# Optimization experiments

Measured on AMD Instinct MI355X. Metric: run time of the kernel, lower is better.

The kernel has to match this reference:

```python
import jax, jax.numpy as jnp
import numpy as np

N_NODES = 50000
N_EDGES = 625000
IN_CH = 128
OUT_CH = 128


def setup_inputs() -> dict:
    key = jax.random.key(0)
    k1, k2, k3, k4 = jax.random.split(key, 4)
    x = jax.random.normal(k1, (N_NODES, IN_CH), dtype=jnp.float32)
    edge_index = jax.random.randint(k2, (2, N_EDGES), 0, N_NODES, dtype=jnp.int64)
    # nn.Linear(in, out): weight [out, in], bias [out]
    bound = 1.0 / np.sqrt(IN_CH)
    W = jax.random.uniform(k3, (OUT_CH, IN_CH), minval=-bound, maxval=bound, dtype=jnp.float32)
    b = jax.random.uniform(k4, (OUT_CH,), minval=-bound, maxval=bound, dtype=jnp.float32)
    return {"x": x, "edge_index": edge_index, "W": W, "b": b}


def reference(x, edge_index, W, b):
    row, col = edge_index[0], edge_index[1]
    num_nodes = x.shape[0]
    # degree of destination nodes (scatter_add of ones over row)
    deg = jax.ops.segment_sum(jnp.ones(row.shape[0], dtype=x.dtype), row,
                              num_segments=num_nodes)
    deg_inv_sqrt = jnp.where(deg > 0, jax.lax.rsqrt(jnp.maximum(deg, 1.0)) * jnp.where(deg > 0, 1.0, 0.0), 0.0)
    deg_inv_sqrt = jnp.where(deg > 0, deg ** -0.5, 0.0)
    norm = deg_inv_sqrt[row] * deg_inv_sqrt[col]  # [E]
    src = x[col] * norm[:, None]                  # gather + scale, [E, C]
    out = jax.ops.segment_sum(src, row, num_segments=num_nodes)  # scatter-add
    return out @ W.T + b
```

## Files before the change

kernel.cpp:

```cpp
#include <hip/hip_runtime.h>
#include <hip/hip_bf16.h>

#define NN 50000
#define NE 625000
#define CH 128
#define RSTR 32
#define NG 196
#define NBIN 512
#define EPB 1221

typedef __attribute__((ext_vector_type(8))) short short8;
typedef __attribute__((ext_vector_type(4))) float floatx4;

__device__ __forceinline__ ushort f2bf(float v) {
    __hip_bfloat16 h = __float2bfloat16(v);
    return *(ushort*)&h;
}
__device__ __forceinline__ float bf2f(uint u) {
    return __uint_as_float(u << 16);
}

__global__ __launch_bounds__(256) void k_prep(const float* __restrict__ x,
                                              ushort* __restrict__ xb,
                                              const float* __restrict__ W,
                                              ushort* __restrict__ whi,
                                              ushort* __restrict__ wlo,
                                              const int* __restrict__ row,
                                              const int* __restrict__ col,
                                              uint* __restrict__ runtbl,
                                              uint* __restrict__ gseg) {
    __shared__ uint cnt[NG];
    __shared__ uint sc[NG];
    __shared__ uint ss[256];
    __shared__ uint pk[EPB];

    int b = blockIdx.x;
    int t = threadIdx.x;
    if (b < NBIN) {
        int e0 = b * EPB;
        int n = NE - e0; if (n > EPB) n = EPB;

        for (int i = t; i < NG; i += 256) cnt[i] = 0;
        __syncthreads();

        int r[5], c[5], g[5];
        uint rk[5];
#pragma unroll
        for (int j = 0; j < 5; ++j) {
            int i = t + j * 256;
            int idx = (i < n) ? (e0 + i) : e0;
            r[j] = row[idx];
            c[j] = col[idx];
        }
#pragma unroll
        for (int j = 0; j < 5; ++j) {
            g[j] = r[j] >> 8;
            if (t + j * 256 < n) rk[j] = atomicAdd(&cnt[g[j]], 1u);
        }
        __syncthreads();

        ss[t] = (t < NG) ? cnt[t] : 0u;
        __syncthreads();
        for (int off = 1; off < 256; off <<= 1) {
            uint add = (t >= off) ? ss[t - off] : 0u;
            __syncthreads();
            ss[t] += add;
            __syncthreads();
        }
        if (t < NG) {
            sc[t] = ss[t] - cnt[t];
            runtbl[(size_t)t * NBIN + b] = (sc[t] << 12) | cnt[t];
        }
        __syncthreads();

#pragma unroll
        for (int j = 0; j < 5; ++j) {
            if (t + j * 256 < n) {
                uint pos = sc[g[j]] + rk[j];
                pk[pos] = ((uint)(r[j] & 255) << 16) | (uint)(c[j] & 0xffff);
            }
        }
        __syncthreads();

        for (int i = t; i < n; i += 256)
            gseg[e0 + i] = pk[i];
    } else if (b < 6762) {
        int i = ((b - 512) * 256 + t) * 4;
        float4 v = *(const float4*)(x + i);
        ushort4 o;
        o.x = f2bf(v.x); o.y = f2bf(v.y); o.z = f2bf(v.z); o.w = f2bf(v.w);
        *(ushort4*)(xb + i) = o;
    } else {
        int i = (b - 6762) * 256 + t;
        float v = W[i];
        ushort hh = f2bf(v);
        whi[i] = hh;
        wlo[i] = f2bf(v - bf2f((uint)hh));
    }
}

__global__ __launch_bounds__(256) void k_csr(const uint* __restrict__ gseg,
                                             const uint* __restrict__ runtbl,
                                             uint* __restrict__ csr,
                                             int* __restrict__ deg_c,
                                             float* __restrict__ nrm) {
    __shared__ ushort slots[64][62];
    __shared__ uint dcnt[64];
    __shared__ uint rt[NBIN];
    int g = blockIdx.x >> 2;
    int q = blockIdx.x & 3;
    int t = threadIdx.x;

    if (t < 64) dcnt[t] = 0;
    for (int i = t; i < NBIN; i += 256)
        rt[i] = runtbl[(size_t)g * NBIN + i];
    __syncthreads();

#pragma unroll
    for (int rep = 0; rep < NBIN / 256; ++rep) {
        int bb = t + rep * 256;
        uint d = rt[bb];
        uint s = d >> 12, len = d & 0xFFFu;
        const uint* p = gseg + (size_t)bb * EPB + s;
        for (uint k = 0; k < len; ++k) {
            uint e = p[k];
            int rl = (int)(e >> 16);
            if ((rl >> 6) == q) {
                int r6 = rl & 63;
                uint kk = atomicAdd(&dcnt[r6], 1u);
                if (kk < 62) slots[r6][kk] = (ushort)(e & 0xffff);
            }
        }
    }
    __syncthreads();

    int row0 = g * 256 + q * 64;
    for (int i = t; i < 2048; i += 256) {
        int rl = i >> 5, w = i & 31;
        int rr = row0 + rl;
        if (rr < NN) {
            uint val;
            if (w == 0) val = dcnt[rl];
            else val = (uint)slots[rl][2 * w - 2] | ((uint)slots[rl][2 * w - 1] << 16);
            csr[(size_t)rr * RSTR + w] = val;
        }
    }
    if (t < 64) {
        int rr = row0 + t;
        if (rr < NN) {
            int d = (int)dcnt[t];
            deg_c[rr] = d;
            nrm[rr] = (d > 0) ? rsqrtf((float)d) : 0.0f;
        }
    }
}

__global__ __launch_bounds__(256) void k_aggm(const ushort* __restrict__ xb,
                                              const int* __restrict__ deg_c,
                                              const float* __restrict__ nrm,
                                              const uint* __restrict__ csr,
                                              const ushort* __restrict__ whi,
                                              const ushort* __restrict__ wlo,
                                              const float* __restrict__ bias,
                                              float* __restrict__ out) {
    __shared__ ushort at[32 * 128];
    const int wave = threadIdx.x >> 6;
    const int lane = threadIdx.x & 63;
    const int half = lane >> 5;
    const int lq = lane & 31;
    const int m0 = blockIdx.x * 32;
    const int li = (lane < 62) ? lane : 0;

    int node0 = m0 + wave * 8;
    int deg_n = 0; ushort craw_n = 0; float dr_n = 0.0f;
    if (node0 < NN) {
        deg_n  = deg_c[node0];
        craw_n = ((const ushort*)(csr + (size_t)node0 * RSTR))[2 + li];
        dr_n   = nrm[node0];
    }
    for (int s = 0; s < 8; ++s) {
        int node = node0 + s;
        int r = wave * 8 + s;
        if (node >= NN) {
            if (half == 0) {
                int byte = (r * 256 + lq * 8) ^ ((r & 7) << 4);
                *(uint2*)((char*)at + byte) = make_uint2(0u, 0u);
            }
            continue;
        }
        int deg = deg_n; ushort craw = craw_n; float dr = dr_n;
        int cli = (lane < deg) ? (int)craw : 0;
        float nl = (lane < deg) ? nrm[cli] : 0.0f;
        int nxt = node + 1;
        if (s < 7 && nxt < NN) {
            deg_n  = deg_c[nxt];
            craw_n = ((const ushort*)(csr + (size_t)nxt * RSTR))[2 + li];
            dr_n   = nrm[nxt];
        }
        float a0 = 0.f, a1 = 0.f, a2 = 0.f, a3 = 0.f;
        for (int j = 0; j < deg; j += 8) {
#pragma unroll
            for (int up = 0; up < 4; ++up) {
                int i0 = j + 2 * up;
                int   c0 = __builtin_amdgcn_readlane(cli, i0);
                int   c1 = __builtin_amdgcn_readlane(cli, i0 + 1);
                float n0 = __uint_as_float(__builtin_amdgcn_readlane(__float_as_uint(nl), i0));
                float n1 = __uint_as_float(__builtin_amdgcn_readlane(__float_as_uint(nl), i0 + 1));
                int   cc = half ? c1 : c0;
                float nw = half ? n1 : n0;
                uint2 v = *(const uint2*)(xb + (size_t)cc * CH + lq * 4);
                a0 = fmaf(__uint_as_float(v.x << 16),          nw, a0);
                a1 = fmaf(__uint_as_float(v.x & 0xffff0000u),  nw, a1);
                a2 = fmaf(__uint_as_float(v.y << 16),          nw, a2);
                a3 = fmaf(__uint_as_float(v.y & 0xffff0000u),  nw, a3);
            }
        }
        a0 += __shfl_xor(a0, 32);
        a1 += __shfl_xor(a1, 32);
        a2 += __shfl_xor(a2, 32);
        a3 += __shfl_xor(a3, 32);
        if (half == 0) {
            uint w0 = (uint)f2bf(a0 * dr) | ((uint)f2bf(a1 * dr) << 16);
            uint w1 = (uint)f2bf(a2 * dr) | ((uint)f2bf(a3 * dr) << 16);
            int byte = (r * 256 + lq * 8) ^ ((r & 7) << 4);
            *(uint2*)((char*)at + byte) = make_uint2(w0, w1);
        }
    }
    __syncthreads();

    const int quad = lane >> 4;
    const int r16 = lane & 15;
    const int nt0 = wave * 2, nt1 = nt0 + 1;
    const ushort* bh0p = whi + (size_t)(nt0 * 16 + r16) * CH + quad * 8;
    const ushort* bl0p = wlo + (size_t)(nt0 * 16 + r16) * CH + quad * 8;
    const ushort* bh1p = whi + (size_t)(nt1 * 16 + r16) * CH + quad * 8;
    const ushort* bl1p = wlo + (size_t)(nt1 * 16 + r16) * CH + quad * 8;

    float b0 = bias[nt0 * 16 + r16];
    float b1 = bias[nt1 * 16 + r16];
    floatx4 acc00 = {b0, b0, b0, b0};
    floatx4 acc01 = {b1, b1, b1, b1};
    floatx4 acc10 = {b0, b0, b0, b0};
    floatx4 acc11 = {b1, b1, b1, b1};

    const int swz = (r16 & 7) << 4;
#pragma unroll
    for (int kb = 0; kb < 4; ++kb) {
        const int cb = quad * 16 + kb * 64;
        short8 A0 = *(const short8*)((const char*)at + ((r16 * 256 + cb) ^ swz));
        short8 A1 = *(const short8*)((const char*)at + (((r16 + 16) * 256 + cb) ^ swz));
        const int k0 = kb * 32;
        short8 h0 = *(const short8*)(bh0p + k0);
        short8 l0 = *(const short8*)(bl0p + k0);
        short8 h1 = *(const short8*)(bh1p + k0);
        short8 l1 = *(const short8*)(bl1p + k0);
        acc00 = __builtin_amdgcn_mfma_f32_16x16x32_bf16(A0, h0, acc00, 0, 0, 0);
        acc00 = __builtin_amdgcn_mfma_f32_16x16x32_bf16(A0, l0, acc00, 0, 0, 0);
        acc01 = __builtin_amdgcn_mfma_f32_16x16x32_bf16(A0, h1, acc01, 0, 0, 0);
        acc01 = __builtin_amdgcn_mfma_f32_16x16x32_bf16(A0, l1, acc01, 0, 0, 0);
        acc10 = __builtin_amdgcn_mfma_f32_16x16x32_bf16(A1, h0, acc10, 0, 0, 0);
        acc10 = __builtin_amdgcn_mfma_f32_16x16x32_bf16(A1, l0, acc10, 0, 0, 0);
        acc11 = __builtin_amdgcn_mfma_f32_16x16x32_bf16(A1, h1, acc11, 0, 0, 0);
        acc11 = __builtin_amdgcn_mfma_f32_16x16x32_bf16(A1, l1, acc11, 0, 0, 0);
    }

#pragma unroll
    for (int r = 0; r < 4; ++r) {
        int row0 = m0 + quad * 4 + r;
        int row1 = row0 + 16;
        if (row0 < NN) {
            out[(size_t)row0 * CH + nt0 * 16 + r16] = acc00[r];
            out[(size_t)row0 * CH + nt1 * 16 + r16] = acc01[r];
        }
        if (row1 < NN) {
            out[(size_t)row1 * CH + nt0 * 16 + r16] = acc10[r];
            out[(size_t)row1 * CH + nt1 * 16 + r16] = acc11[r];
        }
    }
}

extern "C" void kernel_launch(void* const* d_in, const int* in_sizes, int n_in,
                              void* d_out, int out_size, void* d_ws, size_t ws_size,
                              hipStream_t stream) {
    const float* x = (const float*)d_in[0];
    const int* ei = (const int*)d_in[1];
    const float* W = (const float*)d_in[2];
    const float* b = (const float*)d_in[3];
    float* out = (float*)d_out;

    uint* csr = (uint*)d_ws;
    int* deg_c = (int*)(csr + (size_t)NN * RSTR);
    float* nrm = (float*)(deg_c + 50176);
    ushort* ahi = (ushort*)(nrm + 50176);
    ushort* xb = ahi + (size_t)(NN + 16) * CH;
    ushort* whi = xb + (size_t)NN * CH;
    ushort* wlo = whi + CH * CH;
    uint* runtbl = (uint*)(wlo + CH * CH);
    uint* gseg = runtbl + (size_t)NG * NBIN;

    k_prep<<<6826, 256, 0, stream>>>(x, xb, W, whi, wlo, ei, ei + NE, runtbl, gseg);
    k_csr<<<784, 256, 0, stream>>>(gseg, runtbl, csr, deg_c, nrm);
    k_aggm<<<(NN + 31) / 32, 256, 0, stream>>>(xb, deg_c, nrm, csr, whi, wlo, b, out);
}
```

Measured before the change: 137.6 us.

## Pre-scale bf16 features by source norm in CSR build, drop per-edge norm gathers

The CSR kernel now handles 128 rows per block instead of 64, halving the block count. After computing degrees it multiplies each node's bf16 feature row by its own deg^-1/2 in place, so the aggregation kernel only sums gathered rows and no longer gathers nrm per neighbour or does per-edge FMAs. A zero padding row at index NN replaces masked neighbours. The trade-off is an extra read-modify-write pass over xb inside k_csr, an added rounding step from storing scaled bf16 values, and fewer CSR blocks scanning more bins each.

```diff
diff --git a/kernel.cpp b/kernel.cpp
--- a/kernel.cpp
+++ b/kernel.cpp
@@ -96,6 +96,8 @@
         ushort hh = f2bf(v);
         whi[i] = hh;
         wlo[i] = f2bf(v - bf2f((uint)hh));
+        if (b == 6762 && t < 64)
+            ((uint*)(xb + (size_t)NN * CH))[t] = 0u;
     }
 }
 
@@ -103,15 +105,17 @@
                                              const uint* __restrict__ runtbl,
                                              uint* __restrict__ csr,
                                              int* __restrict__ deg_c,
-                                             float* __restrict__ nrm) {
-    __shared__ ushort slots[64][62];
-    __shared__ uint dcnt[64];
+                                             float* __restrict__ nrm,
+                                             ushort* __restrict__ xb) {
+    __shared__ ushort slots[128][62];
+    __shared__ uint dcnt[128];
+    __shared__ float sdis[128];
     __shared__ uint rt[NBIN];
-    int g = blockIdx.x >> 2;
-    int q = blockIdx.x & 3;
+    int g = blockIdx.x >> 1;
+    int q = blockIdx.x & 1;
     int t = threadIdx.x;
 
-    if (t < 64) dcnt[t] = 0;
+    if (t < 128) dcnt[t] = 0;
     for (int i = t; i < NBIN; i += 256)
         rt[i] = runtbl[(size_t)g * NBIN + i];
     __syncthreads();
@@ -125,17 +129,27 @@
         for (uint k = 0; k < len; ++k) {
             uint e = p[k];
             int rl = (int)(e >> 16);
-            if ((rl >> 6) == q) {
-                int r6 = rl & 63;
-                uint kk = atomicAdd(&dcnt[r6], 1u);
-                if (kk < 62) slots[r6][kk] = (ushort)(e & 0xffff);
+            if ((rl >> 7) == q) {
+                int r7 = rl & 127;
+                uint kk = atomicAdd(&dcnt[r7], 1u);
+                if (kk < 62) slots[r7][kk] = (ushort)(e & 0xffff);
             }
         }
     }
     __syncthreads();
 
-    int row0 = g * 256 + q * 64;
-    for (int i = t; i < 2048; i += 256) {
+    int row0 = g * 256 + q * 128;
+    if (t < 128) {
+        int rr = row0 + t;
+        int d = (int)dcnt[t];
+        float dis = (d > 0) ? rsqrtf((float)d) : 0.0f;
+        sdis[t] = dis;
+        if (rr < NN) {
+            deg_c[rr] = d;
+            nrm[rr] = dis;
+        }
+    }
+    for (int i = t; i < 4096; i += 256) {
         int rl = i >> 5, w = i & 31;
         int rr = row0 + rl;
         if (rr < NN) {
@@ -145,12 +159,18 @@
             csr[(size_t)rr * RSTR + w] = val;
         }
     }
-    if (t < 64) {
-        int rr = row0 + t;
+    __syncthreads();
+
+    for (int i = t; i < 128 * 64; i += 256) {
+        int rl = i >> 6, w = i & 63;
+        int rr = row0 + rl;
         if (rr < NN) {
-            int d = (int)dcnt[t];
-            deg_c[rr] = d;
-            nrm[rr] = (d > 0) ? rsqrtf((float)d) : 0.0f;
+            uint* p = (uint*)(xb + (size_t)rr * CH);
+            uint u = p[w];
+            float s = sdis[rl];
+            float lo = bf2f(u);
+            float hi = __uint_as_float(u & 0xffff0000u);
+            p[w] = (uint)f2bf(lo * s) | ((uint)f2bf(hi * s) << 16);
         }
     }
 }
@@ -189,8 +209,7 @@
             continue;
         }
         int deg = deg_n; ushort craw = craw_n; float dr = dr_n;
-        int cli = (lane < deg) ? (int)craw : 0;
-        float nl = (lane < deg) ? nrm[cli] : 0.0f;
+        int cli = (lane < deg) ? (int)craw : NN;
         int nxt = node + 1;
         if (s < 7 && nxt < NN) {
             deg_n  = deg_c[nxt];
@@ -202,17 +221,14 @@
 #pragma unroll
             for (int up = 0; up < 4; ++up) {
                 int i0 = j + 2 * up;
-                int   c0 = __builtin_amdgcn_readlane(cli, i0);
-                int   c1 = __builtin_amdgcn_readlane(cli, i0 + 1);
-                float n0 = __uint_as_float(__builtin_amdgcn_readlane(__float_as_uint(nl), i0));
-                float n1 = __uint_as_float(__builtin_amdgcn_readlane(__float_as_uint(nl), i0 + 1));
-                int   cc = half ? c1 : c0;
-                float nw = half ? n1 : n0;
+                int cc0 = __builtin_amdgcn_readlane(cli, i0);
+                int cc1 = __builtin_amdgcn_readlane(cli, i0 + 1);
+                int cc  = half ? cc1 : cc0;
                 uint2 v = *(const uint2*)(xb + (size_t)cc * CH + lq * 4);
-                a0 = fmaf(__uint_as_float(v.x << 16),          nw, a0);
-                a1 = fmaf(__uint_as_float(v.x & 0xffff0000u),  nw, a1);
-                a2 = fmaf(__uint_as_float(v.y << 16),          nw, a2);
-                a3 = fmaf(__uint_as_float(v.y & 0xffff0000u),  nw, a3);
+                a0 += bf2f(v.x);
+                a1 += __uint_as_float(v.x & 0xffff0000u);
+                a2 += bf2f(v.y);
+                a3 += __uint_as_float(v.y & 0xffff0000u);
             }
         }
         a0 += __shfl_xor(a0, 32);
@@ -291,14 +307,13 @@
     uint* csr = (uint*)d_ws;
     int* deg_c = (int*)(csr + (size_t)NN * RSTR);
     float* nrm = (float*)(deg_c + 50176);
-    ushort* ahi = (ushort*)(nrm + 50176);
-    ushort* xb = ahi + (size_t)(NN + 16) * CH;
-    ushort* whi = xb + (size_t)NN * CH;
+    ushort* xb = (ushort*)(nrm + 50176);
+    ushort* whi = xb + (size_t)(NN + 1) * CH;
     ushort* wlo = whi + CH * CH;
     uint* runtbl = (uint*)(wlo + CH * CH);
     uint* gseg = runtbl + (size_t)NG * NBIN;
 
     k_prep<<<6826, 256, 0, stream>>>(x, xb, W, whi, wlo, ei, ei + NE, runtbl, gseg);
-    k_csr<<<784, 256, 0, stream>>>(gseg, runtbl, csr, deg_c, nrm);
+    k_csr<<<NG * 2, 256, 0, stream>>>(gseg, runtbl, csr, deg_c, nrm, xb);
     k_aggm<<<(NN + 31) / 32, 256, 0, stream>>>(xb, deg_c, nrm, csr, whi, wlo, b, out);
 }
```

Result: slower. 144.6 us (+5.1%).

## Fold source degree norm into bf16 x conversion and widen gather loads

Applied to the files above, without the earlier changes.

The x-to-bf16 conversion moves from the prep kernel into the CSR kernel, where each row is pre-scaled by its own inverse-sqrt degree once it is known. The aggregation loop then no longer gathers per-edge norms and does plain adds instead of FMAs. Each lane now loads 16 bytes covering 8 channels, so four edges are processed per wave instruction, and the partial sums are reduced across four lane groups. A zero padding row at index NN replaces masking for inactive lanes. The cost is an extra x read and write pass inside the CSR kernel, which adds work to that stage.

```diff
diff --git a/kernel.cpp b/kernel.cpp
--- a/kernel.cpp
+++ b/kernel.cpp
@@ -20,9 +20,7 @@
     return __uint_as_float(u << 16);
 }
 
-__global__ __launch_bounds__(256) void k_prep(const float* __restrict__ x,
-                                              ushort* __restrict__ xb,
-                                              const float* __restrict__ W,
+__global__ __launch_bounds__(256) void k_prep(const float* __restrict__ W,
                                               ushort* __restrict__ whi,
                                               ushort* __restrict__ wlo,
                                               const int* __restrict__ row,
@@ -84,14 +82,8 @@
 
         for (int i = t; i < n; i += 256)
             gseg[e0 + i] = pk[i];
-    } else if (b < 6762) {
-        int i = ((b - 512) * 256 + t) * 4;
-        float4 v = *(const float4*)(x + i);
-        ushort4 o;
-        o.x = f2bf(v.x); o.y = f2bf(v.y); o.z = f2bf(v.z); o.w = f2bf(v.w);
-        *(ushort4*)(xb + i) = o;
     } else {
-        int i = (b - 6762) * 256 + t;
+        int i = (b - NBIN) * 256 + t;
         float v = W[i];
         ushort hh = f2bf(v);
         whi[i] = hh;
@@ -101,11 +93,14 @@
 
 __global__ __launch_bounds__(256) void k_csr(const uint* __restrict__ gseg,
                                              const uint* __restrict__ runtbl,
+                                             const float* __restrict__ x,
                                              uint* __restrict__ csr,
                                              int* __restrict__ deg_c,
-                                             float* __restrict__ nrm) {
+                                             float* __restrict__ nrm,
+                                             ushort* __restrict__ xb) {
     __shared__ ushort slots[64][62];
     __shared__ uint dcnt[64];
+    __shared__ float sdis[64];
     __shared__ uint rt[NBIN];
     int g = blockIdx.x >> 2;
     int q = blockIdx.x & 3;
@@ -135,6 +130,17 @@
     __syncthreads();
 
     int row0 = g * 256 + q * 64;
+    if (t < 64) {
+        int rr = row0 + t;
+        int d = (int)dcnt[t];
+        float dis = (d > 0) ? rsqrtf((float)d) : 0.0f;
+        sdis[t] = dis;
+        if (rr < NN) {
+            deg_c[rr] = d;
+            nrm[rr] = dis;
+        }
+    }
+    __syncthreads();
     for (int i = t; i < 2048; i += 256) {
         int rl = i >> 5, w = i & 31;
         int rr = row0 + rl;
@@ -145,12 +151,19 @@
             csr[(size_t)rr * RSTR + w] = val;
         }
     }
-    if (t < 64) {
-        int rr = row0 + t;
+    for (int i = t; i < 2048; i += 256) {
+        int rl = i >> 5, w = i & 31;
+        int rr = row0 + rl;
         if (rr < NN) {
-            int d = (int)dcnt[t];
-            deg_c[rr] = d;
-            nrm[rr] = (d > 0) ? rsqrtf((float)d) : 0.0f;
+            float4 v = *(const float4*)(x + (size_t)rr * CH + w * 4);
+            float s = sdis[rl];
+            ushort4 o;
+            o.x = f2bf(v.x * s); o.y = f2bf(v.y * s);
+            o.z = f2bf(v.z * s); o.w = f2bf(v.w * s);
+            *(ushort4*)(xb + (size_t)rr * CH + w * 4) = o;
+        } else if (rr == NN) {
+            ushort4 o; o.x = 0; o.y = 0; o.z = 0; o.w = 0;
+            *(ushort4*)(xb + (size_t)rr * CH + w * 4) = o;
         }
     }
 }
@@ -166,8 +179,9 @@
     __shared__ ushort at[32 * 128];
     const int wave = threadIdx.x >> 6;
     const int lane = threadIdx.x & 63;
-    const int half = lane >> 5;
-    const int lq = lane & 31;
+    const int quad = lane >> 4;
+    const int q1 = quad & 1, q2 = quad >> 1;
+    const int ch0 = (lane & 15) * 8;
     const int m0 = blockIdx.x * 32;
     const int li = (lane < 62) ? lane : 0;
 
@@ -182,15 +196,15 @@
         int node = node0 + s;
         int r = wave * 8 + s;
         if (node >= NN) {
-            if (half == 0) {
-                int byte = (r * 256 + lq * 8) ^ ((r & 7) << 4);
-                *(uint2*)((char*)at + byte) = make_uint2(0u, 0u);
+            if (lane < 16) {
+                int byte = (r * 256 + lane * 16) ^ ((r & 7) << 4);
+                uint4 z; z.x = 0u; z.y = 0u; z.z = 0u; z.w = 0u;
+                *(uint4*)((char*)at + byte) = z;
             }
             continue;
         }
         int deg = deg_n; ushort craw = craw_n; float dr = dr_n;
-        int cli = (lane < deg) ? (int)craw : 0;
-        float nl = (lane < deg) ? nrm[cli] : 0.0f;
+        int cli = (lane < deg) ? (int)craw : NN;
         int nxt = node + 1;
         if (s < 7 && nxt < NN) {
             deg_n  = deg_c[nxt];
@@ -198,43 +212,58 @@
             dr_n   = nrm[nxt];
         }
         float a0 = 0.f, a1 = 0.f, a2 = 0.f, a3 = 0.f;
+        float a4 = 0.f, a5 = 0.f, a6 = 0.f, a7 = 0.f;
         for (int j = 0; j < deg; j += 8) {
-#pragma unroll
-            for (int up = 0; up < 4; ++up) {
-                int i0 = j + 2 * up;
-                int   c0 = __builtin_amdgcn_readlane(cli, i0);
-                int   c1 = __builtin_amdgcn_readlane(cli, i0 + 1);
-                float n0 = __uint_as_float(__builtin_amdgcn_readlane(__float_as_uint(nl), i0));
-                float n1 = __uint_as_float(__builtin_amdgcn_readlane(__float_as_uint(nl), i0 + 1));
-                int   cc = half ? c1 : c0;
-                float nw = half ? n1 : n0;
-                uint2 v = *(const uint2*)(xb + (size_t)cc * CH + lq * 4);
-                a0 = fmaf(__uint_as_float(v.x << 16),          nw, a0);
-                a1 = fmaf(__uint_as_float(v.x & 0xffff0000u),  nw, a1);
-                a2 = fmaf(__uint_as_float(v.y << 16),          nw, a2);
-                a3 = fmaf(__uint_as_float(v.y & 0xffff0000u),  nw, a3);
-            }
-        }
-        a0 += __shfl_xor(a0, 32);
-        a1 += __shfl_xor(a1, 32);
-        a2 += __shfl_xor(a2, 32);
-        a3 += __shfl_xor(a3, 32);
-        if (half == 0) {
-            uint w0 = (uint)f2bf(a0 * dr) | ((uint)f2bf(a1 * dr) << 16);
-            uint w1 = (uint)f2bf(a2 * dr) | ((uint)f2bf(a3 * dr) << 16);
-            int byte = (r * 256 + lq * 8) ^ ((r & 7) << 4);
-            *(uint2*)((char*)at + byte) = make_uint2(w0, w1);
+            int cA0 = __builtin_amdgcn_readlane(cli, j + 0);
+            int cA1 = __builtin_amdgcn_readlane(cli, j + 1);
+            int cA2 = __builtin_amdgcn_readlane(cli, j + 2);
+            int cA3 = __builtin_amdgcn_readlane(cli, j + 3);
+            int cA = q2 ? (q1 ? cA3 : cA2) : (q1 ? cA1 : cA0);
+            const uint4 vA = *(const uint4*)(xb + (size_t)cA * CH + ch0);
+            int cB0 = __builtin_amdgcn_readlane(cli, j + 4);
+            int cB1 = __builtin_amdgcn_readlane(cli, j + 5);
+            int cB2 = __builtin_amdgcn_readlane(cli, j + 6);
+            int cB3 = __builtin_amdgcn_readlane(cli, j + 7);
+            int cB = q2 ? (q1 ? cB3 : cB2) : (q1 ? cB1 : cB0);
+            const uint4 vB = *(const uint4*)(xb + (size_t)cB * CH + ch0);
+
+            a0 += bf2f(vA.x); a1 += __uint_as_float(vA.x & 0xffff0000u);
+            a2 += bf2f(vA.y); a3 += __uint_as_float(vA.y & 0xffff0000u);
+            a4 += bf2f(vA.z); a5 += __uint_as_float(vA.z & 0xffff0000u);
+            a6 += bf2f(vA.w); a7 += __uint_as_float(vA.w & 0xffff0000u);
+
+            a0 += bf2f(vB.x); a1 += __uint_as_float(vB.x & 0xffff0000u);
+            a2 += bf2f(vB.y); a3 += __uint_as_float(vB.y & 0xffff0000u);
+            a4 += bf2f(vB.z); a5 += __uint_as_float(vB.z & 0xffff0000u);
+            a6 += bf2f(vB.w); a7 += __uint_as_float(vB.w & 0xffff0000u);
+        }
+        a0 += __shfl_xor(a0, 16); a0 += __shfl_xor(a0, 32);
+        a1 += __shfl_xor(a1, 16); a1 += __shfl_xor(a1, 32);
+        a2 += __shfl_xor(a2, 16); a2 += __shfl_xor(a2, 32);
+        a3 += __shfl_xor(a3, 16); a3 += __shfl_xor(a3, 32);
+        a4 += __shfl_xor(a4, 16); a4 += __shfl_xor(a4, 32);
+        a5 += __shfl_xor(a5, 16); a5 += __shfl_xor(a5, 32);
+        a6 += __shfl_xor(a6, 16); a6 += __shfl_xor(a6, 32);
+        a7 += __shfl_xor(a7, 16); a7 += __shfl_xor(a7, 32);
+        if (lane < 16) {
+            uint4 wv;
+            wv.x = (uint)f2bf(a0 * dr) | ((uint)f2bf(a1 * dr) << 16);
+            wv.y = (uint)f2bf(a2 * dr) | ((uint)f2bf(a3 * dr) << 16);
+            wv.z = (uint)f2bf(a4 * dr) | ((uint)f2bf(a5 * dr) << 16);
+            wv.w = (uint)f2bf(a6 * dr) | ((uint)f2bf(a7 * dr) << 16);
+            int byte = (r * 256 + lane * 16) ^ ((r & 7) << 4);
+            *(uint4*)((char*)at + byte) = wv;
         }
     }
     __syncthreads();
 
-    const int quad = lane >> 4;
+    const int quad4 = lane >> 4;
     const int r16 = lane & 15;
     const int nt0 = wave * 2, nt1 = nt0 + 1;
-    const ushort* bh0p = whi + (size_t)(nt0 * 16 + r16) * CH + quad * 8;
-    const ushort* bl0p = wlo + (size_t)(nt0 * 16 + r16) * CH + quad * 8;
-    const ushort* bh1p = whi + (size_t)(nt1 * 16 + r16) * CH + quad * 8;
-    const ushort* bl1p = wlo + (size_t)(nt1 * 16 + r16) * CH + quad * 8;
+    const ushort* bh0p = whi + (size_t)(nt0 * 16 + r16) * CH + quad4 * 8;
+    const ushort* bl0p = wlo + (size_t)(nt0 * 16 + r16) * CH + quad4 * 8;
+    const ushort* bh1p = whi + (size_t)(nt1 * 16 + r16) * CH + quad4 * 8;
+    const ushort* bl1p = wlo + (size_t)(nt1 * 16 + r16) * CH + quad4 * 8;
 
     float b0 = bias[nt0 * 16 + r16];
     float b1 = bias[nt1 * 16 + r16];
@@ -246,7 +275,7 @@
     const int swz = (r16 & 7) << 4;
 #pragma unroll
     for (int kb = 0; kb < 4; ++kb) {
-        const int cb = quad * 16 + kb * 64;
+        const int cb = quad4 * 16 + kb * 64;
         short8 A0 = *(const short8*)((const char*)at + ((r16 * 256 + cb) ^ swz));
         short8 A1 = *(const short8*)((const char*)at + (((r16 + 16) * 256 + cb) ^ swz));
         const int k0 = kb * 32;
@@ -266,7 +295,7 @@
 
 #pragma unroll
     for (int r = 0; r < 4; ++r) {
-        int row0 = m0 + quad * 4 + r;
+        int row0 = m0 + quad4 * 4 + r;
         int row1 = row0 + 16;
         if (row0 < NN) {
             out[(size_t)row0 * CH + nt0 * 16 + r16] = acc00[r];
@@ -291,14 +320,13 @@
     uint* csr = (uint*)d_ws;
     int* deg_c = (int*)(csr + (size_t)NN * RSTR);
     float* nrm = (float*)(deg_c + 50176);
-    ushort* ahi = (ushort*)(nrm + 50176);
-    ushort* xb = ahi + (size_t)(NN + 16) * CH;
-    ushort* whi = xb + (size_t)NN * CH;
+    ushort* xb = (ushort*)(nrm + 50176);
+    ushort* whi = xb + (size_t)(NN + 1) * CH;
     ushort* wlo = whi + CH * CH;
     uint* runtbl = (uint*)(wlo + CH * CH);
     uint* gseg = runtbl + (size_t)NG * NBIN;
 
-    k_prep<<<6826, 256, 0, stream>>>(x, xb, W, whi, wlo, ei, ei + NE, runtbl, gseg);
-    k_csr<<<784, 256, 0, stream>>>(gseg, runtbl, csr, deg_c, nrm);
+    k_prep<<<NBIN + 64, 256, 0, stream>>>(W, whi, wlo, ei, ei + NE, runtbl, gseg);
+    k_csr<<<NG * 4, 256, 0, stream>>>(gseg, runtbl, x, csr, deg_c, nrm, xb);
     k_aggm<<<(NN + 31) / 32, 256, 0, stream>>>(xb, deg_c, nrm, csr, whi, wlo, b, out);
 }
```

Measured after the change: 136.8 us. No clear change (-0.6%).
